# Performance work log

Measured on AMD Instinct MI355X. Metric: run time of the kernel, lower is better.

The kernel has to match this reference:

```python
import jax, jax.numpy as jnp
import numpy as np

ALPHA_LIF = 0.85   # FastLIFCell decay
V_TH = 2.0         # FastLIFCell threshold
ALPHA_LI = 0.9     # FastLICell decay


def setup_inputs() -> dict:
    key = jax.random.key(0)
    k1, k2 = jax.random.split(key)
    # [T, C=1, H, W] spiking input sequence
    x = jax.random.normal(k1, (256, 1, 512, 512), dtype=jnp.float32)
    # learned conv kernel, Conv2d(1,1,5,padding=2,bias=False) -> OIHW [1,1,5,5]
    kernel = jax.random.normal(k2, (1, 1, 5, 5), dtype=jnp.float32) * 0.2
    return {"x": x, "kernel": kernel}


def reference(x, kernel):
    # Conv weights are time-invariant: apply the SAME-padded conv to all
    # timesteps at once (T acts as the batch dim), identical math to the
    # per-step torch conv.
    pad = (kernel.shape[-1] - 1) // 2
    c = jax.lax.conv_general_dilated(
        x, kernel, window_strides=(1, 1),
        padding=[(pad, pad), (pad, pad)],
        dimension_numbers=("NCHW", "OIHW", "NCHW"),
    )  # [T, 1, H, W]

    def step(carry, c_t):
        s1, s2 = carry
        # FastLIF: leaky integrate, fire, soft reset (subtract threshold)
        v = ALPHA_LIF * s1 + c_t
        spk = (v >= V_TH).astype(v.dtype)
        s1_new = v - spk * V_TH
        # FastLI: leaky integrator readout of the spikes
        s2_new = ALPHA_LI * s2 + spk
        return (s1_new, s2_new), s2_new

    s0 = jnp.zeros(x.shape[1:], dtype=x.dtype)  # [1, H, W]
    _, out = jax.lax.scan(step, (s0, s0), c)
    return out  # [T, 1, H, W]
```

## Files before the change

### kernel.cpp

```cpp
#include <hip/hip_runtime.h>


namespace {

constexpr int T_STEPS = 256;
constexpr int H = 512;
constexpr int W = 512;
constexpr int HW = H * W;
constexpr int TW = 64;
constexpr int TH = 8;
constexpr int HALO_W = TW + 4;
constexpr int HALO_H = TH + 4;
constexpr int NLOAD = HALO_W * HALO_H;
constexpr int NTHREADS = 256;

__device__ __forceinline__ void sync_nodrain_vm() {
    __builtin_amdgcn_sched_barrier(0);
    asm volatile("s_waitcnt lgkmcnt(0)");
    __builtin_amdgcn_s_barrier();
    __builtin_amdgcn_sched_barrier(0);
}

__global__ __launch_bounds__(NTHREADS, 2)
void snn_fused(const float* __restrict__ x, const float* __restrict__ kern,
               float* __restrict__ out) {
    #pragma clang fp contract(off)

    __shared__ double smem[2][NLOAD];

    const int tid = threadIdx.x;
    const int w0 = blockIdx.x * TW;
    const int h0 = blockIdx.y * TH;

    double wgt[25];
    #pragma unroll
    for (int i = 0; i < 25; ++i) wgt[i] = (double)kern[i];

    int  goff[4];
    bool gval[4];
    #pragma unroll
    for (int i = 0; i < 4; ++i) {
        int idx = tid + i * NTHREADS;
        int lh = idx / HALO_W;
        int lwp = idx - lh * HALO_W;
        int gh = h0 - 2 + lh;
        int gw = w0 - 2 + lwp;
        goff[i] = gh * W + gw;
        gval[i] = (idx < NLOAD) &&
                  ((unsigned)gh < (unsigned)H) && ((unsigned)gw < (unsigned)W);
    }

    const int lw  = tid & (TW - 1);
    const int lh0 = (tid >> 6) * 2;
    const int gh0 = h0 + lh0;

    double s1a = 0.0, s2a = 0.0;
    double s1b = 0.0, s2b = 0.0;

    float rA[4], rB[4];
    #pragma unroll
    for (int i = 0; i < 4; ++i) { rA[i] = 0.0f; rB[i] = 0.0f; }

    auto issue_loads = [&](int t, float* r) {
        const float* xt = x + (size_t)t * HW;
        #pragma unroll
        for (int i = 0; i < 4; ++i) {
            if (gval[i]) r[i] = xt[goff[i]];
        }
    };

    auto stage_write = [&](double* buf, const float* r) {
        #pragma unroll
        for (int i = 0; i < 4; ++i) {
            int idx = tid + i * NTHREADS;
            if (idx < NLOAD) buf[idx] = (double)r[i];
        }
    };

    auto step = [&](const double* buf, int t) {
        #pragma clang fp contract(off)
        const double* sm = buf + lh0 * HALO_W + lw;
        double acc0 = 0.0, acc1 = 0.0;
        #pragma unroll
        for (int kh = 0; kh < 6; ++kh) {
            const double* row = sm + kh * HALO_W;
            double c0 = row[0], c1 = row[1], c2 = row[2], c3 = row[3], c4 = row[4];
            if (kh < 5) {
                acc0 = __builtin_fma(wgt[kh * 5 + 0], c0, acc0);
                acc0 = __builtin_fma(wgt[kh * 5 + 1], c1, acc0);
                acc0 = __builtin_fma(wgt[kh * 5 + 2], c2, acc0);
                acc0 = __builtin_fma(wgt[kh * 5 + 3], c3, acc0);
                acc0 = __builtin_fma(wgt[kh * 5 + 4], c4, acc0);
            }
            if (kh >= 1) {
                acc1 = __builtin_fma(wgt[(kh - 1) * 5 + 0], c0, acc1);
                acc1 = __builtin_fma(wgt[(kh - 1) * 5 + 1], c1, acc1);
                acc1 = __builtin_fma(wgt[(kh - 1) * 5 + 2], c2, acc1);
                acc1 = __builtin_fma(wgt[(kh - 1) * 5 + 3], c3, acc1);
                acc1 = __builtin_fma(wgt[(kh - 1) * 5 + 4], c4, acc1);
            }
        }

        {
            double v = 0.85 * s1a + acc0;
            double spk = (v >= 2.0) ? 1.0 : 0.0;
            s1a = v - spk * 2.0;
            s2a = 0.9 * s2a + spk;
        }
        {
            double v = 0.85 * s1b + acc1;
            double spk = (v >= 2.0) ? 1.0 : 0.0;
            s1b = v - spk * 2.0;
            s2b = 0.9 * s2b + spk;
        }

        float* outp = out + (size_t)t * HW + (size_t)gh0 * W + (w0 + lw);
        __builtin_nontemporal_store((float)s2a, outp);
        __builtin_nontemporal_store((float)s2b, outp + W);
    };

    issue_loads(0, rA);
    issue_loads(1, rB);
    stage_write(smem[0], rA);
    sync_nodrain_vm();

    for (int tb = 0; tb < 127; ++tb) {
        const int t0 = 2 * tb;

        issue_loads(t0 + 2, rA);
        step(smem[0], t0);
        stage_write(smem[1], rB);
        sync_nodrain_vm();

        issue_loads(t0 + 3, rB);
        step(smem[1], t0 + 1);
        stage_write(smem[0], rA);
        sync_nodrain_vm();
    }

    step(smem[0], 254);
    stage_write(smem[1], rB);
    sync_nodrain_vm();
    step(smem[1], 255);
}

}

extern "C" void kernel_launch(void* const* d_in, const int* in_sizes, int n_in,
                              void* d_out, int out_size, void* d_ws, size_t ws_size,
                              hipStream_t stream) {
    const float* x    = (const float*)d_in[0];
    const float* kern = (const float*)d_in[1];
    float* out        = (float*)d_out;

    dim3 grid(W / TW, H / TH);
    snn_fused<<<grid, dim3(NTHREADS), 0, stream>>>(x, kern, out);
}
```

Baseline: 538.9 us.

## Stage halo tile as float in LDS and compute horizontal pixel pairs per thread

The shared-memory halo buffer now holds float instead of double, halving LDS footprint and write traffic. Each thread now handles two horizontally adjacent pixels rather than two vertically adjacent ones. It reads three float2 values per kernel row (5 rows instead of 6) and widens to double in registers, keeping the double accumulation. The output becomes a single 8-byte non-temporal store per thread. In exchange, each thread adds float-to-double conversions, and LDS reads use 8-byte aligned vector loads with a new lane-to-address pattern.

```diff
diff --git a/kernel.cpp b/kernel.cpp
--- a/kernel.cpp
+++ b/kernel.cpp
@@ -2,6 +2,8 @@
 
 
 namespace {
+
+typedef float f32x2 __attribute__((ext_vector_type(2)));
 
 constexpr int T_STEPS = 256;
 constexpr int H = 512;
@@ -26,7 +28,7 @@
                float* __restrict__ out) {
     #pragma clang fp contract(off)
 
-    __shared__ double smem[2][NLOAD];
+    __shared__ alignas(16) float smem[2][NLOAD];
 
     const int tid = threadIdx.x;
     const int w0 = blockIdx.x * TW;
@@ -41,18 +43,19 @@
     #pragma unroll
     for (int i = 0; i < 4; ++i) {
         int idx = tid + i * NTHREADS;
-        int lh = idx / HALO_W;
-        int lwp = idx - lh * HALO_W;
-        int gh = h0 - 2 + lh;
-        int gw = w0 - 2 + lwp;
+        int lhh = idx / HALO_W;
+        int lww = idx - lhh * HALO_W;
+        int gh = h0 - 2 + lhh;
+        int gw = w0 - 2 + lww;
         goff[i] = gh * W + gw;
         gval[i] = (idx < NLOAD) &&
                   ((unsigned)gh < (unsigned)H) && ((unsigned)gw < (unsigned)W);
     }
 
-    const int lw  = tid & (TW - 1);
-    const int lh0 = (tid >> 6) * 2;
-    const int gh0 = h0 + lh0;
+    const int lwp = (tid & 31) * 2;
+    const int lh  = tid >> 5;
+    const int gh  = h0 + lh;
+    const int gw  = w0 + lwp;
 
     double s1a = 0.0, s2a = 0.0;
     double s1b = 0.0, s2b = 0.0;
@@ -69,36 +72,35 @@
         }
     };
 
-    auto stage_write = [&](double* buf, const float* r) {
+    auto stage_write = [&](float* buf, const float* r) {
         #pragma unroll
         for (int i = 0; i < 4; ++i) {
             int idx = tid + i * NTHREADS;
-            if (idx < NLOAD) buf[idx] = (double)r[i];
+            if (idx < NLOAD) buf[idx] = r[i];
         }
     };
 
-    auto step = [&](const double* buf, int t) {
+    auto step = [&](const float* buf, int t) {
         #pragma clang fp contract(off)
-        const double* sm = buf + lh0 * HALO_W + lw;
+        const float* sm = buf + lh * HALO_W + lwp;
         double acc0 = 0.0, acc1 = 0.0;
         #pragma unroll
-        for (int kh = 0; kh < 6; ++kh) {
-            const double* row = sm + kh * HALO_W;
-            double c0 = row[0], c1 = row[1], c2 = row[2], c3 = row[3], c4 = row[4];
-            if (kh < 5) {
-                acc0 = __builtin_fma(wgt[kh * 5 + 0], c0, acc0);
-                acc0 = __builtin_fma(wgt[kh * 5 + 1], c1, acc0);
-                acc0 = __builtin_fma(wgt[kh * 5 + 2], c2, acc0);
-                acc0 = __builtin_fma(wgt[kh * 5 + 3], c3, acc0);
-                acc0 = __builtin_fma(wgt[kh * 5 + 4], c4, acc0);
-            }
-            if (kh >= 1) {
-                acc1 = __builtin_fma(wgt[(kh - 1) * 5 + 0], c0, acc1);
-                acc1 = __builtin_fma(wgt[(kh - 1) * 5 + 1], c1, acc1);
-                acc1 = __builtin_fma(wgt[(kh - 1) * 5 + 2], c2, acc1);
-                acc1 = __builtin_fma(wgt[(kh - 1) * 5 + 3], c3, acc1);
-                acc1 = __builtin_fma(wgt[(kh - 1) * 5 + 4], c4, acc1);
-            }
+        for (int kh = 0; kh < 5; ++kh) {
+            const f32x2* r2 = reinterpret_cast<const f32x2*>(sm + kh * HALO_W);
+            f32x2 f0 = r2[0], f1 = r2[1], f2 = r2[2];
+            double c0 = (double)f0.x, c1 = (double)f0.y;
+            double c2 = (double)f1.x, c3 = (double)f1.y;
+            double c4 = (double)f2.x, c5 = (double)f2.y;
+            acc0 = __builtin_fma(wgt[kh * 5 + 0], c0, acc0);
+            acc1 = __builtin_fma(wgt[kh * 5 + 0], c1, acc1);
+            acc0 = __builtin_fma(wgt[kh * 5 + 1], c1, acc0);
+            acc1 = __builtin_fma(wgt[kh * 5 + 1], c2, acc1);
+            acc0 = __builtin_fma(wgt[kh * 5 + 2], c2, acc0);
+            acc1 = __builtin_fma(wgt[kh * 5 + 2], c3, acc1);
+            acc0 = __builtin_fma(wgt[kh * 5 + 3], c3, acc0);
+            acc1 = __builtin_fma(wgt[kh * 5 + 3], c4, acc1);
+            acc0 = __builtin_fma(wgt[kh * 5 + 4], c4, acc0);
+            acc1 = __builtin_fma(wgt[kh * 5 + 4], c5, acc1);
         }
 
         {
@@ -114,9 +116,12 @@
             s2b = 0.9 * s2b + spk;
         }
 
-        float* outp = out + (size_t)t * HW + (size_t)gh0 * W + (w0 + lw);
-        __builtin_nontemporal_store((float)s2a, outp);
-        __builtin_nontemporal_store((float)s2b, outp + W);
+        f32x2 o;
+        o.x = (float)s2a;
+        o.y = (float)s2b;
+        f32x2* outp = reinterpret_cast<f32x2*>(
+            out + (size_t)t * HW + (size_t)gh * W + gw);
+        __builtin_nontemporal_store(o, outp);
     };
 
     issue_loads(0, rA);
```

Result: no change. 541.8 us (+0.5%).
